# Kernel optimization log

Measured on AMD Instinct MI355X. Metric: run time of the kernel, lower is better.

Reference implementation:

```python
import jax, jax.numpy as jnp
import numpy as np
import math

NUM_HEADS = 20
HEAD_SIZE = 20  # newssize = 400
NEG_INF = -1e9


def setup_inputs() -> dict:
    key = jax.random.key(0)
    ks = jax.random.split(key, 10)
    B, S, L, V, D, M = 512, 100, 30, 50000, 400, 128
    user_click = jax.random.randint(ks[0], (B, S, L), 0, V)
    seq_len = jax.random.randint(ks[1], (B,), 1, S + 1)  # at least 1 valid click
    sc = 1.0 / math.sqrt(D)
    return {
        "user_click": user_click,
        "seq_len": seq_len,
        "emb_table": jax.random.normal(ks[2], (V, D), jnp.float32) * 0.02,
        "wq": jax.random.normal(ks[3], (D, D), jnp.float32) * sc,
        "wk": jax.random.normal(ks[4], (D, D), jnp.float32) * sc,
        "wv": jax.random.normal(ks[5], (D, D), jnp.float32) * sc,
        "fc1_w": jax.random.normal(ks[6], (D, M), jnp.float32) * sc,
        "fc1_b": jnp.zeros((M,), jnp.float32),
        "fc2_w": jax.random.normal(ks[7], (M, 1), jnp.float32) * (1.0 / math.sqrt(M)),
        "fc2_b": jnp.zeros((1,), jnp.float32),
    }


def reference(user_click, seq_len, emb_table, wq, wk, wv, fc1_w, fc1_b, fc2_w, fc2_b):
    B, S, L = user_click.shape
    D = emb_table.shape[1]
    H, Dh = NUM_HEADS, HEAD_SIZE

    # news encoder: mean-pooled token embeddings -> [B, S, D]
    click = jnp.take(emb_table, user_click.reshape(-1, L), axis=0).mean(axis=1)
    click = click.reshape(B, S, D)

    # mask: valid positions get +1.0 (as in the torch code), invalid -1e9
    valid = jnp.arange(S)[None, :] < seq_len[:, None]  # [B, S]
    mask = jnp.where(valid, 1.0, NEG_INF).astype(click.dtype)

    # multi-head self-attention over history
    q = (click @ wq).reshape(B, S, H, Dh).transpose(0, 2, 1, 3)
    k = (click @ wk).reshape(B, S, H, Dh).transpose(0, 2, 1, 3)
    v = (click @ wv).reshape(B, S, H, Dh).transpose(0, 2, 1, 3)
    logits = jnp.einsum("bhqd,bhkd->bhqk", q, k) / math.sqrt(Dh)
    logits = logits + mask[:, None, None, :]
    attn = jax.nn.softmax(logits, axis=-1)
    ctx = jnp.einsum("bhqk,bhkd->bhqd", attn, v)
    ctx = ctx.transpose(0, 2, 1, 3).reshape(B, S, D)  # [B, S, D]

    # additive attention pooling over history positions
    e = jnp.tanh(ctx @ fc1_w + fc1_b)            # [B, S, M]
    alpha = e @ fc2_w + fc2_b + mask[:, :, None]  # [B, S, 1]
    w = jax.nn.softmax(alpha, axis=1)
    return jnp.sum(w * ctx, axis=1)               # [B, D]
```

## Files before the change

kernel.cpp:

```cpp
#include <hip/hip_runtime.h>
#include <hip/hip_bf16.h>

using u16 = unsigned short;
using u32 = unsigned int;

#define BB 512
#define SS 100
#define LL 30
#define DD 400
#define MM 128
#define HH 20
#define DHH 20
#define SLAB 1024000ull

typedef short v8s __attribute__((ext_vector_type(8)));
typedef float v4f __attribute__((ext_vector_type(4)));

__device__ __forceinline__ float lo2f(u32 u) { return __uint_as_float(u << 16); }
__device__ __forceinline__ float hi2f(u32 u) { return __uint_as_float(u & 0xffff0000u); }
__device__ __forceinline__ float bf2f(u16 h) { return __uint_as_float(((u32)h) << 16); }
__device__ __forceinline__ u16 f2bf(float f) {
  u32 u = __float_as_uint(f);
  u += 0x7fffu + ((u >> 16) & 1u);
  return (u16)(u >> 16);
}
__device__ __forceinline__ u32 packf2(float a, float b) {
  return (u32)f2bf(a) | (((u32)f2bf(b)) << 16);
}

__global__ __launch_bounds__(256) void k_slice(const float* __restrict__ emb,
                                               u32* __restrict__ embS) {
  const int tid = blockIdx.x * 256 + threadIdx.x;
  if (tid >= 10000000) return;
  const int c = tid % 25;
  const int row = (tid / 25) % 50000;
  const int slice = tid / (25 * 50000);
  const float2 v = *(const float2*)&emb[(size_t)row * DD + (slice * 25 + c) * 2];
  embS[tid] = packf2(v.x, v.y);
}

__global__ __launch_bounds__(256) void k_warm(const uint4* __restrict__ embS4,
                                              float* __restrict__ alpha,
                                              float* __restrict__ sink) {
  const int slice = blockIdx.x & 7;
  const int blk = blockIdx.x >> 3;
  const int gid = blockIdx.x * 256 + threadIdx.x;
  const int gstride = gridDim.x * 256;
  for (int i = gid; i < 51200; i += gstride) alpha[i] = 0.f;
  u32 s = 0;
  const int base = slice * 312500;
  for (int i = blk * 256 + threadIdx.x; i < 312500; i += 320 * 256) {
    const uint4 v = embS4[base + i];
    s += v.x ^ v.y ^ v.z ^ v.w;
  }
  if (s == 0x12345678u) sink[0] = 1.f;
}

__global__ __launch_bounds__(256) void k_trans_all(const float* __restrict__ wq,
    const float* __restrict__ wk, const float* __restrict__ wv,
    const float* __restrict__ f1w, u16* __restrict__ wt, u16* __restrict__ wtf) {
  __shared__ float ts[32][33];
  const int z = blockIdx.z;
  const float* src = (z == 0) ? wq : (z == 1) ? wk : (z == 2) ? wv : f1w;
  u16* dst = (z < 3) ? (wt + (size_t)z * 160000) : wtf;
  const int N = (z < 3) ? 400 : 128;
  const int K = 400;
  const int t = threadIdx.x;
  const int n0 = blockIdx.x * 32, k0 = blockIdx.y * 32;
  const int c = t & 31, r8 = t >> 5;
#pragma unroll
  for (int i = 0; i < 4; ++i) {
    const int k = k0 + r8 + i * 8, n = n0 + c;
    ts[r8 + i * 8][c] = (k < K && n < N) ? src[(size_t)k * N + n] : 0.f;
  }
  __syncthreads();
#pragma unroll
  for (int i = 0; i < 4; ++i) {
    const int n = n0 + r8 + i * 8, k = k0 + c;
    if (n < N && k < K) dst[(size_t)n * K + k] = f2bf(ts[c][r8 + i * 8]);
  }
}

__global__ __launch_bounds__(256) void k_embed_s(const int* __restrict__ uc,
                                                 const u32* __restrict__ embS,
                                                 u32* __restrict__ click) {
  __shared__ int sIdx[600];
  const int slice = blockIdx.x & 7;
  const int chunk = blockIdx.x >> 3;
  const int bs0 = chunk * 20;
  const int t = threadIdx.x;
  for (int i = t; i < 600; i += 256) sIdx[i] = uc[(size_t)bs0 * LL + i];
  __syncthreads();
  if (t >= 250) return;
  const int g = t / 25, c = t % 25;
  const u32* base = embS + (size_t)slice * 50000u * 25u + c;
  float a0 = 0.f, a1 = 0.f, b0 = 0.f, b1 = 0.f;
  const int* i0 = &sIdx[g * 30];
  const int* i1 = &sIdx[(g + 10) * 30];
#pragma unroll 6
  for (int l = 0; l < LL; ++l) {
    const u32 v0 = base[(size_t)i0[l] * 25];
    const u32 v1 = base[(size_t)i1[l] * 25];
    a0 += lo2f(v0); a1 += hi2f(v0);
    b0 += lo2f(v1); b1 += hi2f(v1);
  }
  const float s = 1.0f / (float)LL;
  click[(size_t)(bs0 + g) * 200 + slice * 25 + c]      = packf2(a0 * s, a1 * s);
  click[(size_t)(bs0 + g + 10) * 200 + slice * 25 + c] = packf2(b0 * s, b1 * s);
}

__global__ __launch_bounds__(256) void k_qkv_mfma(const u16* __restrict__ A,
    const u16* __restrict__ Wt, u16* __restrict__ qo, u16* __restrict__ ko_,
    u16* __restrict__ vo) {
  __shared__ u16 As[256][40];
  __shared__ u16 Bs[80][40];
  const int t = threadIdx.x;
  const int wave = t >> 6, lane = t & 63;
  const int q = lane >> 4, l16 = lane & 15;
  const int m0 = blockIdx.x * 256;
  const int mat = blockIdx.y / 5, ntile = blockIdx.y % 5;
  const int nb = ntile * 80;
  const u16* Bt = Wt + (size_t)(mat * 400 + nb) * 400;
  u16* O = (mat == 0) ? qo : ((mat == 1) ? ko_ : vo);
  const int mw = wave * 64;

  v4f acc[4][5];
#pragma unroll
  for (int i = 0; i < 4; ++i)
#pragma unroll
    for (int j = 0; j < 5; ++j) acc[i][j] = (v4f){0.f, 0.f, 0.f, 0.f};

  for (int kt = 0; kt < 13; ++kt) {
    const int k0 = kt * 32;
#pragma unroll
    for (int i = 0; i < 4; ++i) {
      const int id = i * 256 + t;
      const int r = id >> 2, ko = (id & 3) * 8;
      uint4 val = make_uint4(0u, 0u, 0u, 0u);
      if (k0 + ko < 400) val = *(const uint4*)&A[(size_t)(m0 + r) * 400 + k0 + ko];
      *(uint4*)&As[r][ko] = val;
    }
#pragma unroll
    for (int i = 0; i < 2; ++i) {
      const int id = i * 256 + t;
      if (id < 320) {
        const int n = id >> 2, ko = (id & 3) * 8;
        uint4 val = make_uint4(0u, 0u, 0u, 0u);
        if (k0 + ko < 400) val = *(const uint4*)&Bt[(size_t)n * 400 + k0 + ko];
        *(uint4*)&Bs[n][ko] = val;
      }
    }
    __syncthreads();
    v8s a[4], b[5];
#pragma unroll
    for (int ms = 0; ms < 4; ++ms) a[ms] = *(const v8s*)&As[mw + ms * 16 + l16][q * 8];
#pragma unroll
    for (int ns = 0; ns < 5; ++ns) b[ns] = *(const v8s*)&Bs[ns * 16 + l16][q * 8];
#pragma unroll
    for (int ms = 0; ms < 4; ++ms)
#pragma unroll
      for (int ns = 0; ns < 5; ++ns)
        acc[ms][ns] = __builtin_amdgcn_mfma_f32_16x16x32_bf16(a[ms], b[ns], acc[ms][ns], 0, 0, 0);
    __syncthreads();
  }
#pragma unroll
  for (int ms = 0; ms < 4; ++ms)
#pragma unroll
    for (int ns = 0; ns < 5; ++ns) {
      const v4f c = acc[ms][ns];
      const int col = nb + ns * 16 + l16;
      const int head = col / 20, dh = col % 20;
      u16* Oh = O + (size_t)head * SLAB + dh;
#pragma unroll
      for (int reg = 0; reg < 4; ++reg) {
        const int m = m0 + mw + ms * 16 + q * 4 + reg;
        Oh[(size_t)m * 20] = f2bf(c[reg]);
      }
    }
}

__global__ __launch_bounds__(256) void k_vt(const u32* __restrict__ vin,
                                            u32* __restrict__ vout) {
  __shared__ u16 Vs[4][100][22];
  const int wave = threadIdx.x >> 6, lane = threadIdx.x & 63;
  const int c = blockIdx.x * 4 + wave;
  const u32* in = vin + (size_t)c * 1000;
  u32* out = vout + (size_t)c * 1000;
  for (int i = lane; i < 1000; i += 64) {
    const int s = i / 10, dp = i % 10;
    *(u32*)&Vs[wave][s][dp * 2] = in[i];
  }
  __syncthreads();
  for (int o = lane; o < 1000; o += 64) {
    const int d = o / 50, sc = o % 50;
    out[o] = (u32)Vs[wave][2 * sc][d] | (((u32)Vs[wave][2 * sc + 1][d]) << 16);
  }
}

__global__ __launch_bounds__(256) void k_attn_mfma(const u16* __restrict__ qg,
    const u16* __restrict__ kg, const u16* __restrict__ vtg,
    const int* __restrict__ seq, u16* __restrict__ ctxg) {
  __shared__ __align__(16) u16 lds[26752];
  const int b = blockIdx.x / HH, h = blockIdx.x % HH;
  const int t = threadIdx.x;
  const int wave = t >> 6, lane = t & 63;
  const int quad = lane >> 4, l16 = lane & 15;
  const int len = seq[b];
  const u32* qb = (const u32*)(qg + (size_t)h * SLAB + (size_t)b * 2000);
  const u32* kb = (const u32*)(kg + (size_t)h * SLAB + (size_t)b * 2000);
  const u32* vb = (const u32*)(vtg + (size_t)(h * 512 + b) * 2000);
  u32* Q32 = (u32*)lds;
  u32* K32 = (u32*)(lds + 2688);
  u32* V32 = (u32*)(lds + 7168);
  u32* S32 = (u32*)(lds + 11520);
  for (int id = t; id < 1344; id += 256) {
    const int r = id / 12, c = id % 12;
    Q32[id] = (r < 100 && c < 10) ? qb[r * 10 + c] : 0u;
  }
  for (int id = t; id < 2240; id += 256) {
    const int r = id / 20, c = id % 20;
    K32[id] = (r < 100 && c < 10) ? kb[r * 10 + c] : 0u;
  }
  for (int id = t; id < 2176; id += 256) {
    const int d = id / 68, c = id % 68;
    V32[id] = (d < 20 && c < 50) ? vb[d * 50 + c] : 0u;
  }
  for (int id = t; id < 896; id += 256) {
    const int r = id >> 3, c = id & 7;
    S32[r * 68 + 56 + c] = 0u;
  }
  __syncthreads();
  const float sc = 0.2236067977499790f;
  for (int mi = 0; mi < 2; ++mi) {
    const int mt = wave + mi * 4;
    if (mt >= 7) break;
    const v8s a = *(const v8s*)&lds[(mt * 16 + l16) * 24 + quad * 8];
    v4f acc[7];
#pragma unroll
    for (int nt = 0; nt < 7; ++nt) {
      const v8s bk = *(const v8s*)&lds[2688 + (nt * 16 + l16) * 40 + quad * 8];
      acc[nt] = __builtin_amdgcn_mfma_f32_16x16x32_bf16(a, bk, (v4f){0.f,0.f,0.f,0.f}, 0, 0, 0);
    }
#pragma unroll
    for (int reg = 0; reg < 4; ++reg) {
      float v[7];
      float mx = -3.0e38f;
#pragma unroll
      for (int nt = 0; nt < 7; ++nt) {
        const int col = nt * 16 + l16;
        v[nt] = acc[nt][reg] * sc + ((col < len) ? 1.0f : -1e9f);
        mx = fmaxf(mx, v[nt]);
      }
#pragma unroll
      for (int o = 1; o < 16; o <<= 1) mx = fmaxf(mx, __shfl_xor(mx, o));
      float sum = 0.f;
#pragma unroll
      for (int nt = 0; nt < 7; ++nt) { v[nt] = __expf(v[nt] - mx); sum += v[nt]; }
#pragma unroll
      for (int o = 1; o < 16; o <<= 1) sum += __shfl_xor(sum, o);
      const float inv = 1.0f / sum;
      const int row = mt * 16 + quad * 4 + reg;
#pragma unroll
      for (int nt = 0; nt < 7; ++nt)
        lds[11520 + row * 136 + nt * 16 + l16] = f2bf(v[nt] * inv);
    }
  }
  __syncthreads();
  u16* cb = ctxg + (size_t)b * SS * DD + h * DHH;
  for (int mi = 0; mi < 2; ++mi) {
    const int mt = wave + mi * 4;
    if (mt >= 7) break;
    v4f o0 = (v4f){0.f,0.f,0.f,0.f}, o1 = o0;
#pragma unroll
    for (int kc = 0; kc < 4; ++kc) {
      const v8s a  = *(const v8s*)&lds[11520 + (mt * 16 + l16) * 136 + kc * 32 + quad * 8];
      const v8s b0 = *(const v8s*)&lds[7168 + l16 * 136 + kc * 32 + quad * 8];
      const v8s b1 = *(const v8s*)&lds[7168 + (16 + l16) * 136 + kc * 32 + quad * 8];
      o0 = __builtin_amdgcn_mfma_f32_16x16x32_bf16(a, b0, o0, 0, 0, 0);
      o1 = __builtin_amdgcn_mfma_f32_16x16x32_bf16(a, b1, o1, 0, 0, 0);
    }
#pragma unroll
    for (int reg = 0; reg < 4; ++reg) {
      const int q = mt * 16 + quad * 4 + reg;
      if (q < 100) {
        cb[(size_t)q * DD + l16] = f2bf(o0[reg]);
        if (l16 < 4) cb[(size_t)q * DD + 16 + l16] = f2bf(o1[reg]);
      }
    }
  }
}

__global__ __launch_bounds__(256) void k_fc1_alpha(const u16* __restrict__ A,
    const u16* __restrict__ Bt, const float* __restrict__ f1b,
    const float* __restrict__ f2w, float* __restrict__ alpha) {
  __shared__ u16 As[128][40];
  __shared__ u16 Bs[64][40];
  const int t = threadIdx.x;
  const int wave = t >> 6, lane = t & 63;
  const int quad = lane >> 4, l16 = lane & 15;
  const int m0 = blockIdx.x * 128;
  const int nb = blockIdx.y * 64;
  const int mw = wave * 32;
  v4f acc[2][4];
#pragma unroll
  for (int i = 0; i < 2; ++i)
#pragma unroll
    for (int j = 0; j < 4; ++j) acc[i][j] = (v4f){0.f, 0.f, 0.f, 0.f};

  for (int kt = 0; kt < 13; ++kt) {
    const int k0 = kt * 32;
#pragma unroll
    for (int i = 0; i < 2; ++i) {
      const int id = i * 256 + t;
      const int r = id >> 2, ko = (id & 3) * 8;
      uint4 val = make_uint4(0u, 0u, 0u, 0u);
      if (k0 + ko < 400) val = *(const uint4*)&A[(size_t)(m0 + r) * 400 + k0 + ko];
      *(uint4*)&As[r][ko] = val;
    }
    {
      const int r = t >> 2, ko = (t & 3) * 8;
      uint4 val = make_uint4(0u, 0u, 0u, 0u);
      if (k0 + ko < 400) val = *(const uint4*)&Bt[(size_t)(nb + r) * 400 + k0 + ko];
      *(uint4*)&Bs[r][ko] = val;
    }
    __syncthreads();
    v8s a[2], b[4];
#pragma unroll
    for (int ms = 0; ms < 2; ++ms) a[ms] = *(const v8s*)&As[mw + ms * 16 + l16][quad * 8];
#pragma unroll
    for (int ns = 0; ns < 4; ++ns) b[ns] = *(const v8s*)&Bs[ns * 16 + l16][quad * 8];
#pragma unroll
    for (int ms = 0; ms < 2; ++ms)
#pragma unroll
      for (int ns = 0; ns < 4; ++ns)
        acc[ms][ns] = __builtin_amdgcn_mfma_f32_16x16x32_bf16(a[ms], b[ns], acc[ms][ns], 0, 0, 0);
    __syncthreads();
  }
  float fwv[4], fbv[4];
#pragma unroll
  for (int ns = 0; ns < 4; ++ns) {
    fwv[ns] = f2w[nb + ns * 16 + l16];
    fbv[ns] = f1b[nb + ns * 16 + l16];
  }
#pragma unroll
  for (int ms = 0; ms < 2; ++ms)
#pragma unroll
    for (int reg = 0; reg < 4; ++reg) {
      float p = 0.f;
#pragma unroll
      for (int ns = 0; ns < 4; ++ns)
        p += tanhf(acc[ms][ns][reg] + fbv[ns]) * fwv[ns];
#pragma unroll
      for (int o = 1; o < 16; o <<= 1) p += __shfl_xor(p, o);
      if (l16 == 0)
        atomicAdd(&alpha[m0 + mw + ms * 16 + quad * 4 + reg], p);
    }
}

__global__ __launch_bounds__(256) void k_pool(const float* __restrict__ alpha,
    const float* __restrict__ f2b, const int* __restrict__ seq,
    const u16* __restrict__ ctxg, float* __restrict__ out) {
  const int b = blockIdx.x;
  const int t = threadIdx.x, w = t >> 6, lane = t & 63;
  __shared__ float wts[SS];
  const int len = seq[b];
  const float bias = f2b[0];
  if (t < SS) wts[t] = alpha[b * SS + t] + bias + ((t < len) ? 1.0f : -1e9f);
  __syncthreads();
  if (w == 0) {
    const float v0 = wts[lane];
    const float v1 = (lane + 64 < SS) ? wts[lane + 64] : -3.0e38f;
    float mx = fmaxf(v0, v1);
#pragma unroll
    for (int o = 32; o > 0; o >>= 1) mx = fmaxf(mx, __shfl_xor(mx, o));
    const float e0 = __expf(v0 - mx);
    const float e1 = (lane + 64 < SS) ? __expf(v1 - mx) : 0.f;
    float sm = e0 + e1;
#pragma unroll
    for (int o = 32; o > 0; o >>= 1) sm += __shfl_xor(sm, o);
    const float inv = 1.0f / sm;
    wts[lane] = e0 * inv;
    if (lane + 64 < SS) wts[lane + 64] = e1 * inv;
  }
  __syncthreads();
  for (int d = t; d < DD; d += 256) {
    float acc = 0.f;
    const u16* cb = ctxg + (size_t)b * SS * DD + d;
    for (int s = 0; s < SS; ++s) acc += wts[s] * bf2f(cb[(size_t)s * DD]);
    out[(size_t)b * DD + d] = acc;
  }
}

extern "C" void kernel_launch(void* const* d_in, const int* in_sizes, int n_in,
                              void* d_out, int out_size, void* d_ws, size_t ws_size,
                              hipStream_t stream) {
  const int*   uc  = (const int*)d_in[0];
  const int*   seq = (const int*)d_in[1];
  const float* emb = (const float*)d_in[2];
  const float* wq  = (const float*)d_in[3];
  const float* wk  = (const float*)d_in[4];
  const float* wv  = (const float*)d_in[5];
  const float* f1w = (const float*)d_in[6];
  const float* f1b = (const float*)d_in[7];
  const float* f2w = (const float*)d_in[8];
  const float* f2b = (const float*)d_in[9];
  float* out = (float*)d_out;

  u16* vt      = (u16*)d_ws;
  u32* embS    = (u32*)d_ws;
  u16* wt      = (u16*)d_ws + 20000000ull;
  u16* wtf     = (u16*)d_ws + 20480000ull;
  u16* click16 = wtf + 51200ull;
  u16* q16     = click16 + 20480000ull;
  u16* k16     = q16 + 20480000ull;
  u16* v16     = k16 + 20480000ull;
  float* alpha = (float*)(v16 + 20480000ull);
  float* sink  = alpha + 51200ull;

  k_slice<<<39063, 256, 0, stream>>>(emb, embS);
  k_trans_all<<<dim3(13, 13, 4), 256, 0, stream>>>(wq, wk, wv, f1w, wt, wtf);
  k_warm<<<2560, 256, 0, stream>>>((const uint4*)embS, alpha, sink);
  k_embed_s<<<20480, 256, 0, stream>>>(uc, embS, (u32*)click16);
  k_qkv_mfma<<<dim3(200, 15), 256, 0, stream>>>(click16, wt, q16, k16, v16);
  k_vt<<<2560, 256, 0, stream>>>((const u32*)v16, (u32*)vt);
  k_attn_mfma<<<BB * HH, 256, 0, stream>>>(q16, k16, vt, seq, click16);
  k_fc1_alpha<<<dim3(400, 2), 256, 0, stream>>>(click16, wtf, f1b, f2w, alpha);
  k_pool<<<BB, 256, 0, stream>>>(alpha, f2b, seq, click16, out);
}
```

Measured before the change: 647.8 us.

## Keep softmax probabilities in registers and feed PV MFMA directly from transposed scores

The attention kernel now computes S^T by swapping the MFMA operands, so each lane holds a full query column. The row softmax then needs only two cross-lane shuffles, and the probabilities are packed straight into the A operand of the PV MFMA. Only K is staged in LDS, while Q and V fragments are loaded from global memory directly into registers. This removes LDS round trips for Q, V and P and one barrier, at the cost of more registers, half-zero-padded MFMA K-dimension work, and possible out-of-range or unaligned loads for the V/Q padding lanes.

```diff
diff --git a/kernel.cpp b/kernel.cpp
--- a/kernel.cpp
+++ b/kernel.cpp
@@ -200,7 +200,7 @@
 __global__ __launch_bounds__(256) void k_attn_mfma(const u16* __restrict__ qg,
     const u16* __restrict__ kg, const u16* __restrict__ vtg,
     const int* __restrict__ seq, u16* __restrict__ ctxg) {
-  __shared__ __align__(16) u16 lds[26752];
+  __shared__ u32 Ks[2240];
   const int b = blockIdx.x / HH, h = blockIdx.x % HH;
   const int t = threadIdx.x;
   const int wave = t >> 6, lane = t & 63;
@@ -209,75 +209,71 @@
   const u32* qb = (const u32*)(qg + (size_t)h * SLAB + (size_t)b * 2000);
   const u32* kb = (const u32*)(kg + (size_t)h * SLAB + (size_t)b * 2000);
   const u32* vb = (const u32*)(vtg + (size_t)(h * 512 + b) * 2000);
-  u32* Q32 = (u32*)lds;
-  u32* K32 = (u32*)(lds + 2688);
-  u32* V32 = (u32*)(lds + 7168);
-  u32* S32 = (u32*)(lds + 11520);
-  for (int id = t; id < 1344; id += 256) {
-    const int r = id / 12, c = id % 12;
-    Q32[id] = (r < 100 && c < 10) ? qb[r * 10 + c] : 0u;
+
+  uint2 vfr[2][7];
+#pragma unroll
+  for (int dt = 0; dt < 2; ++dt) {
+    const int d = dt * 16 + l16;
+#pragma unroll
+    for (int nt = 0; nt < 7; ++nt)
+      vfr[dt][nt] = *(const uint2*)(vb + d * 50 + nt * 8 + quad * 2);
   }
   for (int id = t; id < 2240; id += 256) {
     const int r = id / 20, c = id % 20;
-    K32[id] = (r < 100 && c < 10) ? kb[r * 10 + c] : 0u;
-  }
-  for (int id = t; id < 2176; id += 256) {
-    const int d = id / 68, c = id % 68;
-    V32[id] = (d < 20 && c < 50) ? vb[d * 50 + c] : 0u;
-  }
-  for (int id = t; id < 896; id += 256) {
-    const int r = id >> 3, c = id & 7;
-    S32[r * 68 + 56 + c] = 0u;
-  }
-  __syncthreads();
+    Ks[id] = (r < 100 && c < 10) ? kb[r * 10 + c] : 0u;
+  }
+  __syncthreads();
+
   const float sc = 0.2236067977499790f;
-  for (int mi = 0; mi < 2; ++mi) {
-    const int mt = wave + mi * 4;
-    if (mt >= 7) break;
-    const v8s a = *(const v8s*)&lds[(mt * 16 + l16) * 24 + quad * 8];
-    v4f acc[7];
-#pragma unroll
-    for (int nt = 0; nt < 7; ++nt) {
-      const v8s bk = *(const v8s*)&lds[2688 + (nt * 16 + l16) * 40 + quad * 8];
-      acc[nt] = __builtin_amdgcn_mfma_f32_16x16x32_bf16(a, bk, (v4f){0.f,0.f,0.f,0.f}, 0, 0, 0);
-    }
-#pragma unroll
-    for (int reg = 0; reg < 4; ++reg) {
-      float v[7];
-      float mx = -3.0e38f;
-#pragma unroll
-      for (int nt = 0; nt < 7; ++nt) {
-        const int col = nt * 16 + l16;
-        v[nt] = acc[nt][reg] * sc + ((col < len) ? 1.0f : -1e9f);
-        mx = fmaxf(mx, v[nt]);
-      }
-#pragma unroll
-      for (int o = 1; o < 16; o <<= 1) mx = fmaxf(mx, __shfl_xor(mx, o));
-      float sum = 0.f;
-#pragma unroll
-      for (int nt = 0; nt < 7; ++nt) { v[nt] = __expf(v[nt] - mx); sum += v[nt]; }
-#pragma unroll
-      for (int o = 1; o < 16; o <<= 1) sum += __shfl_xor(sum, o);
-      const float inv = 1.0f / sum;
-      const int row = mt * 16 + quad * 4 + reg;
-#pragma unroll
-      for (int nt = 0; nt < 7; ++nt)
-        lds[11520 + row * 136 + nt * 16 + l16] = f2bf(v[nt] * inv);
-    }
-  }
-  __syncthreads();
   u16* cb = ctxg + (size_t)b * SS * DD + h * DHH;
   for (int mi = 0; mi < 2; ++mi) {
     const int mt = wave + mi * 4;
     if (mt >= 7) break;
-    v4f o0 = (v4f){0.f,0.f,0.f,0.f}, o1 = o0;
-#pragma unroll
-    for (int kc = 0; kc < 4; ++kc) {
-      const v8s a  = *(const v8s*)&lds[11520 + (mt * 16 + l16) * 136 + kc * 32 + quad * 8];
-      const v8s b0 = *(const v8s*)&lds[7168 + l16 * 136 + kc * 32 + quad * 8];
-      const v8s b1 = *(const v8s*)&lds[7168 + (16 + l16) * 136 + kc * 32 + quad * 8];
-      o0 = __builtin_amdgcn_mfma_f32_16x16x32_bf16(a, b0, o0, 0, 0, 0);
-      o1 = __builtin_amdgcn_mfma_f32_16x16x32_bf16(a, b1, o1, 0, 0, 0);
+    const int qrow = mt * 16 + l16;
+    union { uint2 u[2]; v8s v; } qf;
+    qf.u[0] = *(const uint2*)(qb + qrow * 10 + quad * 4);
+    qf.u[1] = *(const uint2*)(qb + qrow * 10 + quad * 4 + 2);
+    v4f acc[7];
+#pragma unroll
+    for (int nt = 0; nt < 7; ++nt) {
+      const v8s kf = *(const v8s*)&Ks[(nt * 16 + l16) * 20 + quad * 4];
+      acc[nt] = __builtin_amdgcn_mfma_f32_16x16x32_bf16(kf, qf.v, (v4f){0.f,0.f,0.f,0.f}, 0, 0, 0);
+    }
+    float mx = -3.0e38f;
+#pragma unroll
+    for (int nt = 0; nt < 7; ++nt)
+#pragma unroll
+      for (int reg = 0; reg < 4; ++reg) {
+        const int k = nt * 16 + quad * 4 + reg;
+        const float v = acc[nt][reg] * sc + ((k < len) ? 1.0f : -1e9f);
+        acc[nt][reg] = v;
+        mx = fmaxf(mx, v);
+      }
+    mx = fmaxf(mx, __shfl_xor(mx, 16));
+    mx = fmaxf(mx, __shfl_xor(mx, 32));
+    float sum = 0.f;
+#pragma unroll
+    for (int nt = 0; nt < 7; ++nt)
+#pragma unroll
+      for (int reg = 0; reg < 4; ++reg) {
+        const float e = __expf(acc[nt][reg] - mx);
+        acc[nt][reg] = e;
+        sum += e;
+      }
+    sum += __shfl_xor(sum, 16);
+    sum += __shfl_xor(sum, 32);
+    const float inv = 1.0f / sum;
+    v4f o0 = (v4f){0.f, 0.f, 0.f, 0.f}, o1 = o0;
+#pragma unroll
+    for (int nt = 0; nt < 7; ++nt) {
+      union { u32 u[4]; v8s v; } pa, vb0, vb1;
+      pa.u[0] = packf2(acc[nt][0] * inv, acc[nt][1] * inv);
+      pa.u[1] = packf2(acc[nt][2] * inv, acc[nt][3] * inv);
+      pa.u[2] = 0u; pa.u[3] = 0u;
+      vb0.u[0] = vfr[0][nt].x; vb0.u[1] = vfr[0][nt].y; vb0.u[2] = 0u; vb0.u[3] = 0u;
+      vb1.u[0] = vfr[1][nt].x; vb1.u[1] = vfr[1][nt].y; vb1.u[2] = 0u; vb1.u[3] = 0u;
+      o0 = __builtin_amdgcn_mfma_f32_16x16x32_bf16(pa.v, vb0.v, o0, 0, 0, 0);
+      o1 = __builtin_amdgcn_mfma_f32_16x16x32_bf16(pa.v, vb1.v, o1, 0, 0, 0);
     }
 #pragma unroll
     for (int reg = 0; reg < 4; ++reg) {
```

Result: faster. 606.4 us (-6.4%).
